# Kernel optimization log

Measured on AMD Instinct MI355X. Metric: run time of the kernel, lower is better.

Reference implementation:

```python
import jax, jax.numpy as jnp
import numpy as np

B, S, W = 64, 512, 16
E, TE, CE, CC = 300, 50, 50, 50
HID, TGT = 256, 16
VOCAB, TAGV, CHARV = 5002, 50, 100
IN = E + TE + CC  # 400


def setup_inputs() -> dict:
    key = jax.random.key(0)
    ks = jax.random.split(key, 24)
    sc = 0.1
    embed_table = (jax.random.normal(ks[0], (VOCAB, E)) * sc).at[0].set(0.0)
    tag_table = (jax.random.normal(ks[1], (TAGV, TE)) * sc).at[0].set(0.0)
    char_table = (jax.random.normal(ks[2], (CHARV, CE)) * sc).at[0].set(0.0)
    return {
        "X": jax.random.randint(ks[3], (B, S), 0, VOCAB),
        "labels_m": jax.random.uniform(ks[4], (B, S)),
        "tags": jax.random.randint(ks[5], (B, S), 0, TAGV),
        "chars": jax.random.randint(ks[6], (B, S, W), 0, CHARV),
        "embed_table": embed_table,
        "tag_table": tag_table,
        "char_table": char_table,
        "conv_w": jax.random.normal(ks[7], (CC, CE, 3)) * sc,
        "conv_b": jax.random.normal(ks[8], (CC,)) * sc,
        "w_ih_f": jax.random.normal(ks[9], (4 * HID, IN)) * sc,
        "w_hh_f": jax.random.normal(ks[10], (4 * HID, HID)) * sc,
        "b_ih_f": jax.random.normal(ks[11], (4 * HID,)) * sc,
        "b_hh_f": jax.random.normal(ks[12], (4 * HID,)) * sc,
        "w_ih_b": jax.random.normal(ks[13], (4 * HID, IN)) * sc,
        "w_hh_b": jax.random.normal(ks[14], (4 * HID, HID)) * sc,
        "b_ih_b": jax.random.normal(ks[15], (4 * HID,)) * sc,
        "b_hh_b": jax.random.normal(ks[16], (4 * HID,)) * sc,
        "fc_w": jax.random.normal(ks[17], (TGT, 2 * HID)) * sc,
        "fc_b": jax.random.normal(ks[18], (TGT,)) * sc,
        "A": jax.random.normal(ks[19], (TGT, TGT)),
        "wd": jax.random.normal(ks[20], (2 * HID,)),
    }


def _lstm_dir(xs, w_ih, w_hh, b_ih, b_hh, reverse):
    # xs: [S, B, IN] ; PyTorch gate order i,f,g,o
    h0 = jnp.zeros((xs.shape[1], w_hh.shape[1]), xs.dtype)

    def step(carry, x):
        h, c = carry
        g = x @ w_ih.T + h @ w_hh.T + (b_ih + b_hh)
        i, f, gg, o = jnp.split(g, 4, axis=-1)
        c = jax.nn.sigmoid(f) * c + jax.nn.sigmoid(i) * jnp.tanh(gg)
        h = jax.nn.sigmoid(o) * jnp.tanh(c)
        return (h, c), h

    _, hs = jax.lax.scan(step, (h0, h0), xs, reverse=reverse)
    return hs


def _features(X, labels_m, tags, chars, embed_table, tag_table, char_table,
              conv_w, conv_b, w_ih_f, w_hh_f, b_ih_f, b_hh_f,
              w_ih_b, w_hh_b, b_ih_b, b_hh_b, fc_w, fc_b, wd):
    embed = embed_table[X]          # [B,S,E]
    tag_embed = tag_table[tags]     # [B,S,TE]
    ce = char_table[chars]          # [B,S,W,CE]
    ce = ce.transpose(0, 3, 1, 2).reshape(B, CE, S * W)  # [B,CE,S*W]
    conv = jax.lax.conv_general_dilated(
        ce, conv_w, window_strides=(1,), padding=((1, 1),),
        dimension_numbers=("NCH", "OIH", "NCH")) + conv_b[None, :, None]
    char_conv = conv.reshape(B, CC, S, W).max(axis=3).transpose(0, 2, 1)  # [B,S,CC]
    feat = jnp.concatenate([embed, tag_embed, char_conv], axis=2)  # [B,S,IN]
    xs = feat.transpose(1, 0, 2)  # [S,B,IN]
    hf = _lstm_dir(xs, w_ih_f, w_hh_f, b_ih_f, b_hh_f, reverse=False)
    hb = _lstm_dir(xs, w_ih_b, w_hh_b, b_ih_b, b_hh_b, reverse=True)
    H = jnp.concatenate([hf, hb], axis=-1).transpose(1, 0, 2)  # [B,S,2H]
    H = H + labels_m[:, :, None] * wd[None, None, :]
    return H @ fc_w.T + fc_b  # [B,S,TGT]


def _viterbi(P, A):
    Xs = P.transpose(1, 0, 2)  # [S,B,T]
    b_idx = jnp.arange(P.shape[0])

    def vstep(delta, x):
        scores = delta[:, :, None] + A[None] + x[:, None, :]  # [B,prev,cur]
        return scores.max(axis=1), (scores.max(axis=1), scores.argmax(axis=1))

    deltaL, (drest, psis) = jax.lax.scan(vstep, Xs[0], Xs[1:])
    deltas = jnp.concatenate([Xs[0][None], drest], axis=0)  # [S,B,T]
    psi_end = deltaL.argmax(axis=1)                          # [B]
    score0 = deltaL[b_idx, psi_end]

    def back(carry, inp):
        tag, sc = carry
        psi_t, delta_t = inp
        prev = psi_t[b_idx, tag]
        return (prev, sc + delta_t[b_idx, prev]), prev

    (_, score), prevs = jax.lax.scan(back, (psi_end, score0),
                                     (psis, deltas[:-1]), reverse=True)
    path = jnp.concatenate([prevs, psi_end[None]], axis=0).T  # [B,S]
    return path, score


def reference(X, labels_m, tags, chars, embed_table, tag_table, char_table,
              conv_w, conv_b, w_ih_f, w_hh_f, b_ih_f, b_hh_f,
              w_ih_b, w_hh_b, b_ih_b, b_hh_b, fc_w, fc_b, A, wd):
    P = _features(X, labels_m, tags, chars, embed_table, tag_table, char_table,
                  conv_w, conv_b, w_ih_f, w_hh_f, b_ih_f, b_hh_f,
                  w_ih_b, w_hh_b, b_ih_b, b_hh_b, fc_w, fc_b, wd)
    return _viterbi(P, A)
```

## Files before the change

### kernel.cpp

```cpp
#include <hip/hip_runtime.h>


#define DEV __device__ __forceinline__
typedef unsigned short u16;
typedef unsigned int   u32;
typedef unsigned char  u8;
typedef signed char    s8;
using short8  = __attribute__((ext_vector_type(8))) short;
using f32x4   = __attribute__((ext_vector_type(4))) float;
using int4v   = __attribute__((ext_vector_type(4))) int;

DEV float bf2f(u16 u){ union{u32 i; float f;} v; v.i = ((u32)u)<<16; return v.f; }
DEV u16 f2bf(float f){ u32 x = __float_as_uint(f); return (u16)((x + 0x7fffu + ((x>>16)&1u)) >> 16); }
DEV float sigf(float x){ return __builtin_amdgcn_rcpf(1.f + __expf(-x)); }
DEV float tanh_f(float x){ return 1.f - 2.f*__builtin_amdgcn_rcpf(__expf(2.f*x) + 1.f); }
DEV float rdlane_f(float v, int l){
  return __uint_as_float(__builtin_amdgcn_readlane(__float_as_uint(v), l));
}

typedef __attribute__((address_space(1))) const u32 GU;
typedef __attribute__((address_space(3))) u32 LU;
DEV void gld_lds16(const void* g, void* l){
  __builtin_amdgcn_global_load_lds((GU*)g, (LU*)l, 16, 0, 0);
}
DEV void bar_l(){
  __builtin_amdgcn_sched_barrier(0);
  asm volatile("s_waitcnt lgkmcnt(0)" ::: "memory");
  __builtin_amdgcn_s_barrier();
  __builtin_amdgcn_sched_barrier(0);
}

static const size_t OFF_GI   = 0;
static const size_t OFF_P    = 0;
static const size_t OFF_DL   = OFF_P  + (size_t)32768*16*4;
static const size_t OFF_PSI  = OFF_DL + (size_t)32768*16*4;
static const size_t OFF_B    = (size_t)134217728;
static const size_t OFF_WIH  = OFF_B    + (size_t)33554432;
static const size_t OFF_WQ   = OFF_WIH  + (size_t)1703936;
static const size_t OFF_SC   = OFF_WQ   + (size_t)524288;
static const size_t OFF_BIAS = OFF_SC   + 8192;
static const size_t OFF_WFC  = OFF_BIAS + 8192;
static const size_t REQUIRED = OFF_WFC  + 256;

__global__ __launch_bounds__(256) void k0_all(
    const float* __restrict__ whhf, const float* __restrict__ whhb,
    s8* __restrict__ wq, float* __restrict__ sc2,
    const float* bihf, const float* bhhf, const float* bihb, const float* bhhb,
    const float* fcw, const float* wdp, float* bias, float* wfc,
    const float* __restrict__ wihf, const float* __restrict__ wihb, u16* __restrict__ wih)
{
  __shared__ float red[256];
  const int tid = threadIdx.x;
  const int bx = blockIdx.x;
  if (bx > 512){
    const int n = bx - 513;
    const float* src = (n < 1024) ? (wihf + (size_t)n*400) : (wihb + (size_t)(n-1024)*400);
    u32* dst = (u32*)(wih + (size_t)n*416);
    if (tid < 208){
      int j = tid*2;
      u32 v = 0u;
      if (j < 400){
        float2 f = *(const float2*)(src + j);
        v = (u32)f2bf(f.x) | ((u32)f2bf(f.y) << 16);
      }
      dst[tid] = v;
    }
    return;
  }
  if (bx == 512){
    for (int n = tid; n < 2048; n += 256){
      bias[n] = (n < 1024) ? (bihf[n] + bhhf[n]) : (bihb[n-1024] + bhhb[n-1024]);
    }
    const int cur = tid & 15, part = tid >> 4;
    float s = 0.f;
    for (int k = part*32; k < part*32 + 32; k++) s += fcw[cur*512 + k] * wdp[k];
    red[tid] = s;
    __syncthreads();
    if (tid < 16){
      float t = 0.f;
      #pragma unroll
      for (int p = 0; p < 16; p++) t += red[p*16 + tid];
      wfc[tid] = t;
    }
    return;
  }
  const int row = bx*4 + (tid >> 6);
  const int lane = tid & 63;
  const float* src = (row < 1024) ? (whhf + (size_t)row*256)
                                  : (whhb + (size_t)(row-1024)*256);
  f32x4 v = *(const f32x4*)(src + lane*4);
  float m = fmaxf(fmaxf(fabsf(v[0]), fabsf(v[1])), fmaxf(fabsf(v[2]), fabsf(v[3])));
  #pragma unroll
  for (int d = 1; d < 64; d <<= 1) m = fmaxf(m, __shfl_xor(m, d, 64));
  float inv = 127.f / (m + 1e-30f);
  u32 pack = 0;
  #pragma unroll
  for (int e = 0; e < 4; e++){
    int q = (int)rintf(v[e]*inv);
    q = q > 127 ? 127 : (q < -127 ? -127 : q);
    pack |= ((u32)(u8)(s8)q) << (8*e);
  }
  const int dir = row >> 10, n = row & 1023;
  const int g = n >> 8, j = n & 255, w2 = j >> 4, lr2 = j & 15;
  const int kk = lane >> 4, lq2 = (lane >> 2) & 3, e4 = lane & 3;
  u32* wq32 = (u32*)wq;
  wq32[dir*65536 + (((g*16 + w2)*4 + kk)*64 + lq2*16 + lr2)*4 + e4] = pack;
  if (lane == 0) sc2[row] = m * (1.f/16129.f);
}

__global__ __launch_bounds__(256) void k1_feat(
    const int* __restrict__ X, const int* __restrict__ tg, const int* __restrict__ ch,
    const float* __restrict__ etab, const float* __restrict__ ttab, const float* __restrict__ ctab,
    const float* __restrict__ cw, const float* __restrict__ cb, u16* __restrict__ feat)
{
  const int b = blockIdx.y, tid = threadIdx.x;
  __shared__ float ce_s[66*60];
  __shared__ float w_s[150*52];
  for (int i = tid; i < 7500; i += 256){
    int cc = i/150, r2 = i - cc*150;
    int ce = r2/3, dc = r2 - ce*3;
    w_s[(cc*3 + dc)*52 + ce] = cw[i];
  }
  const int li = tid & 15, jg = tid >> 4;

  for (int it = 0; it < 8; it++){
    const int sb = blockIdx.x*8 + it;
    __syncthreads();
    for (int i = tid; i < 600; i += 256){
      int wl = i/150, j = i - wl*150;
      int s = sb*4 + wl;
      int idx = X[b*512 + s];
      float2 f = *(const float2*)(etab + (size_t)idx*300 + j*2);
      *(u32*)(feat + (size_t)(s*64 + b)*416 + j*2) = (u32)f2bf(f.x) | ((u32)f2bf(f.y) << 16);
    }
    for (int i = tid; i < 100; i += 256){
      int wl = i/25, j = i - wl*25;
      int s = sb*4 + wl;
      int idx = tg[b*512 + s];
      float2 f = *(const float2*)(ttab + (size_t)idx*50 + j*2);
      *(u32*)(feat + (size_t)(s*64 + b)*416 + 300 + j*2) = (u32)f2bf(f.x) | ((u32)f2bf(f.y) << 16);
    }
    if (tid < 32){
      int wl = tid>>3, j = tid&7;
      int s = sb*4 + wl;
      *(u32*)(feat + (size_t)(s*64 + b)*416 + 400 + j*2) = 0u;
    }
    for (int i = tid; i < 3300; i += 256){
      int qq = i/50, ce = i - qq*50;
      int p = sb*64 - 1 + qq;
      float v = 0.f;
      if (p >= 0 && p < 8192){
        int ci = ch[b*8192 + p];
        v = ctab[ci*50 + ce];
      }
      ce_s[qq*60 + ce] = v;
    }
    __syncthreads();
    float acc[4][3];
    #pragma unroll
    for (int k=0;k<4;k++){ acc[k][0]=0.f; acc[k][1]=0.f; acc[k][2]=0.f; }
    #pragma unroll
    for (int dc = 0; dc < 3; dc++){
      for (int ceb = 0; ceb < 48; ceb += 4){
        f32x4 w0 = *(const f32x4*)&w_s[((3*jg+0)*3 + dc)*52 + ceb];
        f32x4 w1 = *(const f32x4*)&w_s[((3*jg+1)*3 + dc)*52 + ceb];
        f32x4 w2 = *(const f32x4*)&w_s[((3*jg+2)*3 + dc)*52 + ceb];
        #pragma unroll
        for (int k = 0; k < 4; k++){
          f32x4 cv = *(const f32x4*)&ce_s[(16*k + li + dc)*60 + ceb];
          #pragma unroll
          for (int e = 0; e < 4; e++){
            acc[k][0] += cv[e]*w0[e];
            acc[k][1] += cv[e]*w1[e];
            acc[k][2] += cv[e]*w2[e];
          }
        }
      }
      float w0a = w_s[((3*jg+0)*3+dc)*52 + 48], w0b = w_s[((3*jg+0)*3+dc)*52 + 49];
      float w1a = w_s[((3*jg+1)*3+dc)*52 + 48], w1b = w_s[((3*jg+1)*3+dc)*52 + 49];
      float w2a = w_s[((3*jg+2)*3+dc)*52 + 48], w2b = w_s[((3*jg+2)*3+dc)*52 + 49];
      #pragma unroll
      for (int k = 0; k < 4; k++){
        float ca = ce_s[(16*k + li + dc)*60 + 48];
        float cb2 = ce_s[(16*k + li + dc)*60 + 49];
        acc[k][0] += ca*w0a + cb2*w0b;
        acc[k][1] += ca*w1a + cb2*w1b;
        acc[k][2] += ca*w2a + cb2*w2b;
      }
    }
    #pragma unroll
    for (int m = 1; m < 16; m <<= 1)
      #pragma unroll
      for (int k=0;k<4;k++)
        #pragma unroll
        for (int c=0;c<3;c++)
          acc[k][c] = fmaxf(acc[k][c], __shfl_xor(acc[k][c], m, 64));
    if (li == 0){
      #pragma unroll
      for (int k=0;k<4;k++)
        #pragma unroll
        for (int c=0;c<3;c++){
          int cc = 3*jg + c;
          int s = sb*4 + k;
          feat[(size_t)(s*64 + b)*416 + 350 + cc] = f2bf(acc[k][c] + cb[cc]);
        }
    }
    if (tid < 128){
      int pl = tid & 63, cc = 48 + (tid >> 6);
      float a2 = 0.f;
      #pragma unroll
      for (int dc = 0; dc < 3; dc++){
        for (int ceb = 0; ceb < 48; ceb += 4){
          f32x4 wv = *(const f32x4*)&w_s[(cc*3 + dc)*52 + ceb];
          f32x4 cv = *(const f32x4*)&ce_s[(pl + dc)*60 + ceb];
          a2 += cv[0]*wv[0] + cv[1]*wv[1] + cv[2]*wv[2] + cv[3]*wv[3];
        }
        a2 += ce_s[(pl+dc)*60 + 48]*w_s[(cc*3+dc)*52 + 48]
            + ce_s[(pl+dc)*60 + 49]*w_s[(cc*3+dc)*52 + 49];
      }
      #pragma unroll
      for (int m = 1; m < 16; m <<= 1) a2 = fmaxf(a2, __shfl_xor(a2, m, 64));
      if ((tid & 15) == 0){
        int s = sb*4 + ((tid & 63) >> 4);
        feat[(size_t)(s*64 + b)*416 + 350 + cc] = f2bf(a2 + cb[cc]);
      }
    }
  }
}

__global__ __launch_bounds__(256) void k2_gemm(
    const u16* __restrict__ featp, const u16* __restrict__ wihp,
    const float* __restrict__ bias, u16* __restrict__ gi)
{
  const int m0 = blockIdx.y*128, n0 = blockIdx.x*128;
  const int tid = threadIdx.x, wv = tid>>6, lane = tid&63;
  const int lr = lane & 15, lq = lane >> 4;
  const int wm = (wv>>1)*64, wn = (wv&1)*64;
  __shared__ u16 As[2][4096], Bs[2][4096];
  f32x4 acc[4][4];
  #pragma unroll
  for (int a=0;a<4;a++)
    #pragma unroll
    for (int c=0;c<4;c++) acc[a][c] = (f32x4){0.f,0.f,0.f,0.f};

  const size_t arow = (size_t)(m0 + ((wv)*16) + (lane>>2))*416 + (lane&3)*8;
  const size_t brow = (size_t)(n0 + ((wv)*16) + (lane>>2))*416 + (lane&3)*8;
  #define K2_STAGE(BUF, K0) { \
    _Pragma("unroll") \
    for (int i = 0; i < 2; i++){ \
      int c = i*4 + wv; \
      gld_lds16(featp + (size_t)(m0 + c*16 + (lane>>2))*416 + (K0) + (lane&3)*8, &As[BUF][c*512]); \
      gld_lds16(wihp  + (size_t)(n0 + c*16 + (lane>>2))*416 + (K0) + (lane&3)*8, &Bs[BUF][c*512]); \
    } }

  K2_STAGE(0, 0);
  __syncthreads();
  int buf = 0;
  for (int ki = 0; ki < 13; ki++){
    if (ki < 12) K2_STAGE(buf^1, (ki+1)*32);
    short8 af[4], bfr[4];
    #pragma unroll
    for (int mt=0; mt<4; mt++) af[mt]  = *(const short8*)(&As[buf][0] + (wm + mt*16 + lr)*32 + lq*8);
    #pragma unroll
    for (int nt=0; nt<4; nt++) bfr[nt] = *(const short8*)(&Bs[buf][0] + (wn + nt*16 + lr)*32 + lq*8);
    #pragma unroll
    for (int mt=0; mt<4; mt++)
      #pragma unroll
      for (int nt=0; nt<4; nt++)
        acc[mt][nt] = __builtin_amdgcn_mfma_f32_16x16x32_bf16(af[mt], bfr[nt], acc[mt][nt], 0,0,0);
    __syncthreads();
    buf ^= 1;
  }
  #undef K2_STAGE
  (void)arow; (void)brow;
  #pragma unroll
  for (int nt=0; nt<4; nt++){
    float bv = bias[n0 + wn + nt*16 + lr];
    #pragma unroll
    for (int mt=0; mt<4; mt++)
      #pragma unroll
      for (int r=0; r<4; r++)
        gi[(size_t)(m0 + wm + mt*16 + lq*4 + r)*2048 + n0 + wn + nt*16 + lr]
            = f2bf(acc[mt][nt][r] + bv);
  }
}

__global__ __launch_bounds__(512, 2) void k3_lstm(
    const s8* __restrict__ wq, const float* __restrict__ sc2,
    const u16* __restrict__ gi, u16* __restrict__ hcat)
{
  const int dir = blockIdx.x >> 5;
  const int bb  = (blockIdx.x & 31) * 2;
  const int tid = threadIdx.x;
  const int w = tid >> 6, lane = tid & 63;
  const int lr = lane & 15, lq = lane >> 4;
  const int cb = tid >> 8, cj = tid & 255;

  __shared__ s8 Hs[2][4096];
  __shared__ float xbuf[2048];

  const s8* wqd = wq + dir*262144;
  int4v bq[2][4][4];
  #pragma unroll
  for (int sl = 0; sl < 2; sl++)
    #pragma unroll
    for (int g = 0; g < 4; g++)
      #pragma unroll
      for (int kk = 0; kk < 4; kk++)
        bq[sl][g][kk] = *(const int4v*)(wqd + (((((g*16 + 2*w + sl)*4 + kk)*64) + lane) << 4));

  float scl[4];
  #pragma unroll
  for (int g = 0; g < 4; g++) scl[g] = sc2[dir*1024 + g*256 + cj];

  *(uint2*)&Hs[0][tid*8] = (uint2){0u,0u};
  *(uint2*)&Hs[1][tid*8] = (uint2){0u,0u};

  float cst = 0.f;
  const ptrdiff_t dstep = dir ? -(ptrdiff_t)131072 : (ptrdiff_t)131072;
  const u16* g0 = gi + (size_t)((dir ? 511 : 0)*64 + bb + cb)*2048 + dir*1024 + cj;
  u32 gcur[4], gn1[4], gn2[4];
  #pragma unroll
  for (int g = 0; g < 4; g++) gcur[g] = g0[g*256];
  const u16* g1 = g0 + dstep;
  #pragma unroll
  for (int g = 0; g < 4; g++) gn1[g] = g1[g*256];
  const u16* gpref = g1;
  __syncthreads();

  #pragma unroll 1
  for (int t = 0; t < 512; t++){
    const int s = dir ? (511 - t) : t;
    if (t + 2 < 512) gpref += dstep;
    #pragma unroll
    for (int g = 0; g < 4; g++) gn2[g] = gpref[g*256];
    const s8* hb = Hs[t & 1];
    int4v aq[4];
    #pragma unroll
    for (int kk = 0; kk < 4; kk++)
      aq[kk] = *(const int4v*)(hb + lr*256 + ((kk*64 + lq*16) ^ (lr << 4)));
    int4v acc[2][4];
    #pragma unroll
    for (int sl = 0; sl < 2; sl++)
      #pragma unroll
      for (int g = 0; g < 4; g++) acc[sl][g] = (int4v){0,0,0,0};
    __builtin_amdgcn_s_setprio(1);
    #pragma unroll
    for (int kk = 0; kk < 4; kk++)
      #pragma unroll
      for (int sl = 0; sl < 2; sl++)
        #pragma unroll
        for (int g = 0; g < 4; g++)
          acc[sl][g] = __builtin_amdgcn_mfma_i32_16x16x64_i8(aq[kk], bq[sl][g][kk], acc[sl][g], 0,0,0);
    __builtin_amdgcn_s_setprio(0);
    if (lq == 0){
      #pragma unroll
      for (int sl = 0; sl < 2; sl++){
        const int j = (2*w + sl)*16 + lr;
        #pragma unroll
        for (int r = 0; r < 2; r++){
          f32x4 v = (f32x4){(float)acc[sl][0][r], (float)acc[sl][1][r],
                            (float)acc[sl][2][r], (float)acc[sl][3][r]};
          *(f32x4*)&xbuf[(r*256 + j)*4] = v;
        }
      }
    }
    bar_l();
    f32x4 p = *(const f32x4*)&xbuf[tid*4];
    float g4[4];
    #pragma unroll
    for (int g = 0; g < 4; g++) g4[g] = bf2f((u16)gcur[g]) + p[g]*scl[g];
    float iv = sigf(g4[0]), fv = sigf(g4[1]);
    float gg = tanh_f(g4[2]), ov = sigf(g4[3]);
    float c = fv*cst + iv*gg;
    cst = c;
    float h = ov * tanh_f(c);
    hcat[(size_t)(s*64 + bb + cb)*512 + dir*256 + cj] = f2bf(h);
    Hs[(t + 1) & 1][cb*256 + (cj ^ (cb << 4))] = (s8)(int)rintf(h * 127.f);
    #pragma unroll
    for (int g = 0; g < 4; g++){ gcur[g] = gn1[g]; gn1[g] = gn2[g]; }
    bar_l();
  }
}

__global__ __launch_bounds__(256) void k4_fc(
    const u16* __restrict__ hcat, const float* __restrict__ fcw, const float* __restrict__ fcb,
    const float* __restrict__ lmp, const float* __restrict__ wfc, float* __restrict__ Pout)
{
  const int wv = threadIdx.x >> 6, lane = threadIdx.x & 63;
  const int lr = lane & 15, lq = lane >> 4;
  const int mt = blockIdx.x*4 + wv;
  short8 bfr[16];
  #pragma unroll
  for (int kk = 0; kk < 16; kk++){
    const float* wr = fcw + (size_t)lr*512 + kk*32 + lq*8;
    f32x4 w0 = *(const f32x4*)wr;
    f32x4 w1 = *(const f32x4*)(wr + 4);
    short8 sv;
    #pragma unroll
    for (int e = 0; e < 4; e++){ sv[e] = (short)f2bf(w0[e]); sv[4+e] = (short)f2bf(w1[e]); }
    bfr[kk] = sv;
  }
  f32x4 acc = (f32x4){0.f,0.f,0.f,0.f};
  #pragma unroll
  for (int kk = 0; kk < 16; kk++){
    short8 af = *(const short8*)(hcat + (size_t)(mt*16 + lr)*512 + kk*32 + lq*8);
    acc = __builtin_amdgcn_mfma_f32_16x16x32_bf16(af, bfr[kk], acc, 0,0,0);
  }
  const int cur = lr;
  float fb = fcb[cur];
  float wf = wfc[cur];
  #pragma unroll
  for (int r = 0; r < 4; r++){
    int m = mt*16 + lq*4 + r;
    int b = m & 63, s = m >> 6;
    float lmv = lmp[b*512 + s];
    Pout[(size_t)m*16 + cur] = acc[r] + fb + lmv*wf;
  }
}

__global__ __launch_bounds__(64) void k5_vit(
    const float* __restrict__ Pg, const float* __restrict__ Am,
    float* __restrict__ dout, float* __restrict__ dl, u8* __restrict__ psi)
{
  const int b = blockIdx.x, lane = threadIdx.x;
  const int cur = lane & 15;
  float Ar[16];
  #pragma unroll
  for (int p = 0; p < 16; p++) Ar[p] = Am[p*16 + cur];
  float dreg[16];
  {
    float v0 = Pg[(size_t)b*16 + cur];
    if (lane < 16) dl[(size_t)b*16 + cur] = v0;
    #pragma unroll
    for (int c = 0; c < 16; c++) dreg[c] = rdlane_f(v0, c);
  }

#define FSTEP(X, S) { \
    float v_[16]; \
    _Pragma("unroll") \
    for (int p = 0; p < 16; p++) v_[p] = dreg[p] + Ar[p]; \
    float m1[8]; int i1[8]; \
    _Pragma("unroll") \
    for (int k = 0; k < 8; k++){ bool c_ = v_[2*k] >= v_[2*k+1]; \
      m1[k] = c_ ? v_[2*k] : v_[2*k+1]; i1[k] = c_ ? 2*k : 2*k+1; } \
    float m2[4]; int i2[4]; \
    _Pragma("unroll") \
    for (int k = 0; k < 4; k++){ bool c_ = m1[2*k] >= m1[2*k+1]; \
      m2[k] = c_ ? m1[2*k] : m1[2*k+1]; i2[k] = c_ ? i1[2*k] : i1[2*k+1]; } \
    float m3[2]; int i3[2]; \
    _Pragma("unroll") \
    for (int k = 0; k < 2; k++){ bool c_ = m2[2*k] >= m2[2*k+1]; \
      m3[k] = c_ ? m2[2*k] : m2[2*k+1]; i3[k] = c_ ? i2[2*k] : i2[2*k+1]; } \
    bool cf_ = m3[0] >= m3[1]; \
    float best = (cf_ ? m3[0] : m3[1]) + (X); \
    int bi = cf_ ? i3[0] : i3[1]; \
    if (lane < 16){ \
      dl[(size_t)((S)*64 + b)*16 + cur] = best; \
      psi[(size_t)((S)*64 + b)*16 + cur] = (u8)bi; \
    } \
    _Pragma("unroll") \
    for (int c = 0; c < 16; c++) dreg[c] = rdlane_f(best, c); \
  }

  float x0 = Pg[(size_t)(1*64 + b)*16 + cur];
  float x1 = Pg[(size_t)(2*64 + b)*16 + cur];
  float x2 = Pg[(size_t)(3*64 + b)*16 + cur];
  float x3 = Pg[(size_t)(4*64 + b)*16 + cur];
  for (int s = 1; s < 512; s += 4){
    FSTEP(x0, s);
    if (s + 4 < 512) x0 = Pg[(size_t)((s+4)*64 + b)*16 + cur];
    if (s + 1 < 512) FSTEP(x1, s+1);
    if (s + 5 < 512) x1 = Pg[(size_t)((s+5)*64 + b)*16 + cur];
    if (s + 2 < 512) FSTEP(x2, s+2);
    if (s + 6 < 512) x2 = Pg[(size_t)((s+6)*64 + b)*16 + cur];
    if (s + 3 < 512) FSTEP(x3, s+3);
    if (s + 7 < 512) x3 = Pg[(size_t)((s+7)*64 + b)*16 + cur];
  }
#undef FSTEP

  float bv = dreg[0]; int bix = 0;
  #pragma unroll
  for (int c = 1; c < 16; c++){ if (dreg[c] > bv){ bv = dreg[c]; bix = c; } }
  int tag = bix;
  float score = bv;
  if (lane == 0) dout[b*512 + 511] = (float)tag;

#define BSTEP(PV, DV, T) { \
    int prev = __builtin_amdgcn_readlane((PV), tag); \
    score += rdlane_f((DV), prev); \
    if (lane == 0) dout[b*512 + (T)] = (float)prev; \
    tag = prev; }

  int   p0 = 0, p1 = 0, p2 = 0, p3 = 0;
  float d0 = 0.f, d1 = 0.f, d2 = 0.f, d3 = 0.f;
  if (lane < 16){
    p0 = psi[(size_t)(511*64 + b)*16 + lane]; d0 = dl[(size_t)(510*64 + b)*16 + lane];
    p1 = psi[(size_t)(510*64 + b)*16 + lane]; d1 = dl[(size_t)(509*64 + b)*16 + lane];
    p2 = psi[(size_t)(509*64 + b)*16 + lane]; d2 = dl[(size_t)(508*64 + b)*16 + lane];
    p3 = psi[(size_t)(508*64 + b)*16 + lane]; d3 = dl[(size_t)(507*64 + b)*16 + lane];
  }
  for (int t = 510; t >= 0; t -= 4){
    BSTEP(p0, d0, t);
    if (t - 4 >= 0 && lane < 16){
      p0 = psi[(size_t)((t-3)*64 + b)*16 + lane]; d0 = dl[(size_t)((t-4)*64 + b)*16 + lane];
    }
    if (t - 1 >= 0) BSTEP(p1, d1, t-1);
    if (t - 5 >= 0 && lane < 16){
      p1 = psi[(size_t)((t-4)*64 + b)*16 + lane]; d1 = dl[(size_t)((t-5)*64 + b)*16 + lane];
    }
    if (t - 2 >= 0) BSTEP(p2, d2, t-2);
    if (t - 6 >= 0 && lane < 16){
      p2 = psi[(size_t)((t-5)*64 + b)*16 + lane]; d2 = dl[(size_t)((t-6)*64 + b)*16 + lane];
    }
    if (t - 3 >= 0) BSTEP(p3, d3, t-3);
    if (t - 7 >= 0 && lane < 16){
      p3 = psi[(size_t)((t-6)*64 + b)*16 + lane]; d3 = dl[(size_t)((t-7)*64 + b)*16 + lane];
    }
  }
#undef BSTEP
  if (lane == 0) dout[32768 + b] = score;
}

extern "C" void kernel_launch(void* const* d_in, const int* in_sizes, int n_in,
                              void* d_out, int out_size, void* d_ws, size_t ws_size,
                              hipStream_t stream)
{
  (void)in_sizes; (void)n_in; (void)out_size;
  if (ws_size < REQUIRED) return;

  const int*   X    = (const int*)d_in[0];
  const float* lm   = (const float*)d_in[1];
  const int*   tg   = (const int*)d_in[2];
  const int*   ch   = (const int*)d_in[3];
  const float* etab = (const float*)d_in[4];
  const float* ttab = (const float*)d_in[5];
  const float* ctab = (const float*)d_in[6];
  const float* cw   = (const float*)d_in[7];
  const float* cb   = (const float*)d_in[8];
  const float* wihf = (const float*)d_in[9];
  const float* whhf = (const float*)d_in[10];
  const float* bihf = (const float*)d_in[11];
  const float* bhhf = (const float*)d_in[12];
  const float* wihb = (const float*)d_in[13];
  const float* whhb = (const float*)d_in[14];
  const float* bihb = (const float*)d_in[15];
  const float* bhhb = (const float*)d_in[16];
  const float* fcw  = (const float*)d_in[17];
  const float* fcb  = (const float*)d_in[18];
  const float* Am   = (const float*)d_in[19];
  const float* wdp  = (const float*)d_in[20];

  char* ws = (char*)d_ws;
  u16*   gi   = (u16*)(ws + OFF_GI);
  u16*   feat = (u16*)(ws + OFF_B);
  u16*   hcat = (u16*)(ws + OFF_B);
  u16*   wih  = (u16*)(ws + OFF_WIH);
  s8*    wq   = (s8*)(ws + OFF_WQ);
  float* sc2  = (float*)(ws + OFF_SC);
  float* Pg   = (float*)(ws + OFF_P);
  float* dlt  = (float*)(ws + OFF_DL);
  u8*    psi  = (u8*)(ws + OFF_PSI);
  float* bias = (float*)(ws + OFF_BIAS);
  float* wfc  = (float*)(ws + OFF_WFC);
  float* dout = (float*)d_out;

  k0_all<<<2561, 256, 0, stream>>>(whhf, whhb, wq, sc2,
                                   bihf, bhhf, bihb, bhhb, fcw, wdp, bias, wfc,
                                   wihf, wihb, wih);
  k1_feat<<<dim3(16, 64), 256, 0, stream>>>(X, tg, ch, etab, ttab, ctab, cw, cb, feat);
  k2_gemm<<<dim3(16, 256), 256, 0, stream>>>(feat, wih, bias, gi);
  k3_lstm<<<64, 512, 0, stream>>>(wq, sc2, gi, hcat);
  k4_fc<<<512, 256, 0, stream>>>(hcat, fcw, fcb, lm, wfc, Pg);
  k5_vit<<<64, 64, 0, stream>>>(Pg, Am, dout, dlt, psi);
}
```

Before: 1.074 ms.

## Fuse weight prep and feature kernels; split embedding gather and prefetch char gathers

New measurement: 1.072 ms. About the same (-0.2%).

```diff
diff --git a/kernel.cpp b/kernel.cpp
--- a/kernel.cpp
+++ b/kernel.cpp
@@ -12,6 +12,7 @@
 
 DEV float bf2f(u16 u){ union{u32 i; float f;} v; v.i = ((u32)u)<<16; return v.f; }
 DEV u16 f2bf(float f){ u32 x = __float_as_uint(f); return (u16)((x + 0x7fffu + ((x>>16)&1u)) >> 16); }
+DEV u32 pk2(float a, float b){ return (u32)f2bf(a) | ((u32)f2bf(b) << 16); }
 DEV float sigf(float x){ return __builtin_amdgcn_rcpf(1.f + __expf(-x)); }
 DEV float tanh_f(float x){ return 1.f - 2.f*__builtin_amdgcn_rcpf(__expf(2.f*x) + 1.f); }
 DEV float rdlane_f(float v, int l){
@@ -42,16 +43,163 @@
 static const size_t OFF_WFC  = OFF_BIAS + 8192;
 static const size_t REQUIRED = OFF_WFC  + 256;
 
-__global__ __launch_bounds__(256) void k0_all(
+__global__ __launch_bounds__(256) void k01_fused(
+    const int* __restrict__ X, const int* __restrict__ tg, const int* __restrict__ ch,
+    const float* __restrict__ etab, const float* __restrict__ ttab, const float* __restrict__ ctab,
+    const float* __restrict__ cw, const float* __restrict__ cb, u16* __restrict__ feat,
     const float* __restrict__ whhf, const float* __restrict__ whhb,
     s8* __restrict__ wq, float* __restrict__ sc2,
     const float* bihf, const float* bhhf, const float* bihb, const float* bhhb,
     const float* fcw, const float* wdp, float* bias, float* wfc,
     const float* __restrict__ wihf, const float* __restrict__ wihb, u16* __restrict__ wih)
 {
-  __shared__ float red[256];
+  __shared__ float smem[3960 + 7800];
   const int tid = threadIdx.x;
-  const int bx = blockIdx.x;
+  const int bid = blockIdx.x;
+
+  if (bid < 1024){
+    float* ce_s = smem;
+    float* w_s  = smem + 3960;
+    const int b = bid >> 4, sbb = bid & 15;
+    for (int i = tid; i < 7500; i += 256){
+      int cc = i/150, r2 = i - cc*150;
+      int ce = r2/3, dc = r2 - ce*3;
+      w_s[(cc*3 + dc)*52 + ce] = cw[i];
+    }
+    const int li = tid & 15, jg = tid >> 4;
+    float stg[13];
+
+    #define GATHER(T) { \
+      const int sbg = sbb*8 + (T); \
+      _Pragma("unroll") \
+      for (int j = 0; j < 13; j++){ \
+        int i = tid + 256*j; \
+        float v = 0.f; \
+        if (i < 3300){ \
+          int qq = i/50, ce = i - qq*50; \
+          int p = sbg*64 - 1 + qq; \
+          if (p >= 0 && p < 8192){ int ci = ch[b*8192 + p]; v = ctab[ci*50 + ce]; } \
+        } \
+        stg[j] = v; \
+      } }
+
+    GATHER(0);
+    for (int t = 0; t < 8; t++){
+      const int sb = sbb*8 + t;
+      bar_l();
+      #pragma unroll
+      for (int j = 0; j < 13; j++){
+        int i = tid + 256*j;
+        if (i < 3300){
+          int qq = i/50, ce = i - qq*50;
+          ce_s[qq*60 + ce] = stg[j];
+        }
+      }
+      bar_l();
+      if (t < 7) GATHER(t+1);
+
+      float acc[4][3];
+      #pragma unroll
+      for (int k=0;k<4;k++){ acc[k][0]=0.f; acc[k][1]=0.f; acc[k][2]=0.f; }
+      #pragma unroll
+      for (int dc = 0; dc < 3; dc++){
+        for (int ceb = 0; ceb < 48; ceb += 4){
+          f32x4 w0 = *(const f32x4*)&w_s[((3*jg+0)*3 + dc)*52 + ceb];
+          f32x4 w1 = *(const f32x4*)&w_s[((3*jg+1)*3 + dc)*52 + ceb];
+          f32x4 w2 = *(const f32x4*)&w_s[((3*jg+2)*3 + dc)*52 + ceb];
+          #pragma unroll
+          for (int k = 0; k < 4; k++){
+            f32x4 cv = *(const f32x4*)&ce_s[(16*k + li + dc)*60 + ceb];
+            #pragma unroll
+            for (int e = 0; e < 4; e++){
+              acc[k][0] += cv[e]*w0[e];
+              acc[k][1] += cv[e]*w1[e];
+              acc[k][2] += cv[e]*w2[e];
+            }
+          }
+        }
+        float w0a = w_s[((3*jg+0)*3+dc)*52 + 48], w0b = w_s[((3*jg+0)*3+dc)*52 + 49];
+        float w1a = w_s[((3*jg+1)*3+dc)*52 + 48], w1b = w_s[((3*jg+1)*3+dc)*52 + 49];
+        float w2a = w_s[((3*jg+2)*3+dc)*52 + 48], w2b = w_s[((3*jg+2)*3+dc)*52 + 49];
+        #pragma unroll
+        for (int k = 0; k < 4; k++){
+          float ca  = ce_s[(16*k + li + dc)*60 + 48];
+          float cb2 = ce_s[(16*k + li + dc)*60 + 49];
+          acc[k][0] += ca*w0a + cb2*w0b;
+          acc[k][1] += ca*w1a + cb2*w1b;
+          acc[k][2] += ca*w2a + cb2*w2b;
+        }
+      }
+      #pragma unroll
+      for (int m = 1; m < 16; m <<= 1)
+        #pragma unroll
+        for (int k=0;k<4;k++)
+          #pragma unroll
+          for (int c=0;c<3;c++)
+            acc[k][c] = fmaxf(acc[k][c], __shfl_xor(acc[k][c], m, 64));
+      if (li == 0){
+        #pragma unroll
+        for (int k=0;k<4;k++)
+          #pragma unroll
+          for (int c=0;c<3;c++){
+            int cc = 3*jg + c;
+            int s = sb*4 + k;
+            feat[(size_t)(s*64 + b)*416 + 350 + cc] = f2bf(acc[k][c] + cb[cc]);
+          }
+      }
+      if (tid < 128){
+        int pl = tid & 63, cc = 48 + (tid >> 6);
+        float a2 = 0.f;
+        #pragma unroll
+        for (int dc = 0; dc < 3; dc++){
+          for (int ceb = 0; ceb < 48; ceb += 4){
+            f32x4 wv = *(const f32x4*)&w_s[(cc*3 + dc)*52 + ceb];
+            f32x4 cv = *(const f32x4*)&ce_s[(pl + dc)*60 + ceb];
+            a2 += cv[0]*wv[0] + cv[1]*wv[1] + cv[2]*wv[2] + cv[3]*wv[3];
+          }
+          a2 += ce_s[(pl+dc)*60 + 48]*w_s[(cc*3+dc)*52 + 48]
+              + ce_s[(pl+dc)*60 + 49]*w_s[(cc*3+dc)*52 + 49];
+        }
+        #pragma unroll
+        for (int m = 1; m < 16; m <<= 1) a2 = fmaxf(a2, __shfl_xor(a2, m, 64));
+        if ((tid & 15) == 0){
+          int s = sb*4 + ((tid & 63) >> 4);
+          feat[(size_t)(s*64 + b)*416 + 350 + cc] = f2bf(a2 + cb[cc]);
+        }
+      }
+    }
+    #undef GATHER
+    return;
+  }
+
+  if (bid < 3072){
+    const int cid = bid - 1024;
+    const int w = tid >> 6, lane = tid & 63;
+    #pragma unroll
+    for (int r = 0; r < 4; r++){
+      const int m = cid*16 + w*4 + r;
+      const int s = m >> 6, b = m & 63;
+      const int xi = X[b*512 + s];
+      const int ti = tg[b*512 + s];
+      u32* dst = (u32*)feat + (size_t)m*208;
+      #pragma unroll
+      for (int pass = 0; pass < 3; pass++){
+        int word = pass*64 + lane;
+        if (word < 150){
+          float2 f = *(const float2*)(etab + (size_t)xi*300 + word*2);
+          dst[word] = pk2(f.x, f.y);
+        } else if (word < 175){
+          float2 f = *(const float2*)(ttab + (size_t)ti*50 + (word-150)*2);
+          dst[word] = pk2(f.x, f.y);
+        } else if (word < 183){
+          dst[200 + word - 175] = 0u;
+        }
+      }
+    }
+    return;
+  }
+
+  const int bx = bid - 3072;
   if (bx > 512){
     const int n = bx - 513;
     const float* src = (n < 1024) ? (wihf + (size_t)n*400) : (wihb + (size_t)(n-1024)*400);
@@ -61,13 +209,14 @@
       u32 v = 0u;
       if (j < 400){
         float2 f = *(const float2*)(src + j);
-        v = (u32)f2bf(f.x) | ((u32)f2bf(f.y) << 16);
+        v = pk2(f.x, f.y);
       }
       dst[tid] = v;
     }
     return;
   }
   if (bx == 512){
+    float* red = smem;
     for (int n = tid; n < 2048; n += 256){
       bias[n] = (n < 1024) ? (bihf[n] + bhhf[n]) : (bihb[n-1024] + bhhb[n-1024]);
     }
@@ -84,147 +233,29 @@
     }
     return;
   }
-  const int row = bx*4 + (tid >> 6);
-  const int lane = tid & 63;
-  const float* src = (row < 1024) ? (whhf + (size_t)row*256)
-                                  : (whhb + (size_t)(row-1024)*256);
-  f32x4 v = *(const f32x4*)(src + lane*4);
-  float m = fmaxf(fmaxf(fabsf(v[0]), fabsf(v[1])), fmaxf(fabsf(v[2]), fabsf(v[3])));
-  #pragma unroll
-  for (int d = 1; d < 64; d <<= 1) m = fmaxf(m, __shfl_xor(m, d, 64));
-  float inv = 127.f / (m + 1e-30f);
-  u32 pack = 0;
-  #pragma unroll
-  for (int e = 0; e < 4; e++){
-    int q = (int)rintf(v[e]*inv);
-    q = q > 127 ? 127 : (q < -127 ? -127 : q);
-    pack |= ((u32)(u8)(s8)q) << (8*e);
-  }
-  const int dir = row >> 10, n = row & 1023;
-  const int g = n >> 8, j = n & 255, w2 = j >> 4, lr2 = j & 15;
-  const int kk = lane >> 4, lq2 = (lane >> 2) & 3, e4 = lane & 3;
-  u32* wq32 = (u32*)wq;
-  wq32[dir*65536 + (((g*16 + w2)*4 + kk)*64 + lq2*16 + lr2)*4 + e4] = pack;
-  if (lane == 0) sc2[row] = m * (1.f/16129.f);
-}
-
-__global__ __launch_bounds__(256) void k1_feat(
-    const int* __restrict__ X, const int* __restrict__ tg, const int* __restrict__ ch,
-    const float* __restrict__ etab, const float* __restrict__ ttab, const float* __restrict__ ctab,
-    const float* __restrict__ cw, const float* __restrict__ cb, u16* __restrict__ feat)
-{
-  const int b = blockIdx.y, tid = threadIdx.x;
-  __shared__ float ce_s[66*60];
-  __shared__ float w_s[150*52];
-  for (int i = tid; i < 7500; i += 256){
-    int cc = i/150, r2 = i - cc*150;
-    int ce = r2/3, dc = r2 - ce*3;
-    w_s[(cc*3 + dc)*52 + ce] = cw[i];
-  }
-  const int li = tid & 15, jg = tid >> 4;
-
-  for (int it = 0; it < 8; it++){
-    const int sb = blockIdx.x*8 + it;
-    __syncthreads();
-    for (int i = tid; i < 600; i += 256){
-      int wl = i/150, j = i - wl*150;
-      int s = sb*4 + wl;
-      int idx = X[b*512 + s];
-      float2 f = *(const float2*)(etab + (size_t)idx*300 + j*2);
-      *(u32*)(feat + (size_t)(s*64 + b)*416 + j*2) = (u32)f2bf(f.x) | ((u32)f2bf(f.y) << 16);
-    }
-    for (int i = tid; i < 100; i += 256){
-      int wl = i/25, j = i - wl*25;
-      int s = sb*4 + wl;
-      int idx = tg[b*512 + s];
-      float2 f = *(const float2*)(ttab + (size_t)idx*50 + j*2);
-      *(u32*)(feat + (size_t)(s*64 + b)*416 + 300 + j*2) = (u32)f2bf(f.x) | ((u32)f2bf(f.y) << 16);
-    }
-    if (tid < 32){
-      int wl = tid>>3, j = tid&7;
-      int s = sb*4 + wl;
-      *(u32*)(feat + (size_t)(s*64 + b)*416 + 400 + j*2) = 0u;
-    }
-    for (int i = tid; i < 3300; i += 256){
-      int qq = i/50, ce = i - qq*50;
-      int p = sb*64 - 1 + qq;
-      float v = 0.f;
-      if (p >= 0 && p < 8192){
-        int ci = ch[b*8192 + p];
-        v = ctab[ci*50 + ce];
-      }
-      ce_s[qq*60 + ce] = v;
-    }
-    __syncthreads();
-    float acc[4][3];
-    #pragma unroll
-    for (int k=0;k<4;k++){ acc[k][0]=0.f; acc[k][1]=0.f; acc[k][2]=0.f; }
-    #pragma unroll
-    for (int dc = 0; dc < 3; dc++){
-      for (int ceb = 0; ceb < 48; ceb += 4){
-        f32x4 w0 = *(const f32x4*)&w_s[((3*jg+0)*3 + dc)*52 + ceb];
-        f32x4 w1 = *(const f32x4*)&w_s[((3*jg+1)*3 + dc)*52 + ceb];
-        f32x4 w2 = *(const f32x4*)&w_s[((3*jg+2)*3 + dc)*52 + ceb];
-        #pragma unroll
-        for (int k = 0; k < 4; k++){
-          f32x4 cv = *(const f32x4*)&ce_s[(16*k + li + dc)*60 + ceb];
-          #pragma unroll
-          for (int e = 0; e < 4; e++){
-            acc[k][0] += cv[e]*w0[e];
-            acc[k][1] += cv[e]*w1[e];
-            acc[k][2] += cv[e]*w2[e];
-          }
-        }
-      }
-      float w0a = w_s[((3*jg+0)*3+dc)*52 + 48], w0b = w_s[((3*jg+0)*3+dc)*52 + 49];
-      float w1a = w_s[((3*jg+1)*3+dc)*52 + 48], w1b = w_s[((3*jg+1)*3+dc)*52 + 49];
-      float w2a = w_s[((3*jg+2)*3+dc)*52 + 48], w2b = w_s[((3*jg+2)*3+dc)*52 + 49];
-      #pragma unroll
-      for (int k = 0; k < 4; k++){
-        float ca = ce_s[(16*k + li + dc)*60 + 48];
-        float cb2 = ce_s[(16*k + li + dc)*60 + 49];
-        acc[k][0] += ca*w0a + cb2*w0b;
-        acc[k][1] += ca*w1a + cb2*w1b;
-        acc[k][2] += ca*w2a + cb2*w2b;
-      }
-    }
-    #pragma unroll
-    for (int m = 1; m < 16; m <<= 1)
-      #pragma unroll
-      for (int k=0;k<4;k++)
-        #pragma unroll
-        for (int c=0;c<3;c++)
-          acc[k][c] = fmaxf(acc[k][c], __shfl_xor(acc[k][c], m, 64));
-    if (li == 0){
-      #pragma unroll
-      for (int k=0;k<4;k++)
-        #pragma unroll
-        for (int c=0;c<3;c++){
-          int cc = 3*jg + c;
-          int s = sb*4 + k;
-          feat[(size_t)(s*64 + b)*416 + 350 + cc] = f2bf(acc[k][c] + cb[cc]);
-        }
-    }
-    if (tid < 128){
-      int pl = tid & 63, cc = 48 + (tid >> 6);
-      float a2 = 0.f;
-      #pragma unroll
-      for (int dc = 0; dc < 3; dc++){
-        for (int ceb = 0; ceb < 48; ceb += 4){
-          f32x4 wv = *(const f32x4*)&w_s[(cc*3 + dc)*52 + ceb];
-          f32x4 cv = *(const f32x4*)&ce_s[(pl + dc)*60 + ceb];
-          a2 += cv[0]*wv[0] + cv[1]*wv[1] + cv[2]*wv[2] + cv[3]*wv[3];
-        }
-        a2 += ce_s[(pl+dc)*60 + 48]*w_s[(cc*3+dc)*52 + 48]
-            + ce_s[(pl+dc)*60 + 49]*w_s[(cc*3+dc)*52 + 49];
-      }
-      #pragma unroll
-      for (int m = 1; m < 16; m <<= 1) a2 = fmaxf(a2, __shfl_xor(a2, m, 64));
-      if ((tid & 15) == 0){
-        int s = sb*4 + ((tid & 63) >> 4);
-        feat[(size_t)(s*64 + b)*416 + 350 + cc] = f2bf(a2 + cb[cc]);
-      }
-    }
+  {
+    const int row = bx*4 + (tid >> 6);
+    const int lane = tid & 63;
+    const float* src = (row < 1024) ? (whhf + (size_t)row*256)
+                                    : (whhb + (size_t)(row-1024)*256);
+    f32x4 v = *(const f32x4*)(src + lane*4);
+    float m = fmaxf(fmaxf(fabsf(v[0]), fabsf(v[1])), fmaxf(fabsf(v[2]), fabsf(v[3])));
+    #pragma unroll
+    for (int d = 1; d < 64; d <<= 1) m = fmaxf(m, __shfl_xor(m, d, 64));
+    float inv = 127.f / (m + 1e-30f);
+    u32 pack = 0;
+    #pragma unroll
+    for (int e = 0; e < 4; e++){
+      int q = (int)rintf(v[e]*inv);
+      q = q > 127 ? 127 : (q < -127 ? -127 : q);
+      pack |= ((u32)(u8)(s8)q) << (8*e);
+    }
+    const int dir = row >> 10, n = row & 1023;
+    const int g = n >> 8, j = n & 255, w2 = j >> 4, lr2 = j & 15;
+    const int kk = lane >> 4, lq2 = (lane >> 2) & 3, e4 = lane & 3;
+    u32* wq32 = (u32*)wq;
+    wq32[dir*65536 + (((g*16 + w2)*4 + kk)*64 + lq2*16 + lr2)*4 + e4] = pack;
+    if (lane == 0) sc2[row] = m * (1.f/16129.f);
   }
 }
 
@@ -243,8 +274,6 @@
     #pragma unroll
     for (int c=0;c<4;c++) acc[a][c] = (f32x4){0.f,0.f,0.f,0.f};
 
-  const size_t arow = (size_t)(m0 + ((wv)*16) + (lane>>2))*416 + (lane&3)*8;
-  const size_t brow = (size_t)(n0 + ((wv)*16) + (lane>>2))*416 + (lane&3)*8;
   #define K2_STAGE(BUF, K0) { \
     _Pragma("unroll") \
     for (int i = 0; i < 2; i++){ \
@@ -272,7 +301,6 @@
     buf ^= 1;
   }
   #undef K2_STAGE
-  (void)arow; (void)brow;
   #pragma unroll
   for (int nt=0; nt<4; nt++){
     float bv = bias[n0 + wn + nt*16 + lr];
@@ -565,10 +593,10 @@
   float* wfc  = (float*)(ws + OFF_WFC);
   float* dout = (float*)d_out;
 
-  k0_all<<<2561, 256, 0, stream>>>(whhf, whhb, wq, sc2,
-                                   bihf, bhhf, bihb, bhhb, fcw, wdp, bias, wfc,
-                                   wihf, wihb, wih);
-  k1_feat<<<dim3(16, 64), 256, 0, stream>>>(X, tg, ch, etab, ttab, ctab, cw, cb, feat);
+  k01_fused<<<5633, 256, 0, stream>>>(X, tg, ch, etab, ttab, ctab, cw, cb, feat,
+                                      whhf, whhb, wq, sc2,
+                                      bihf, bhhf, bihb, bhhb, fcw, wdp, bias, wfc,
+                                      wihf, wihb, wih);
   k2_gemm<<<dim3(16, 256), 256, 0, stream>>>(feat, wih, bias, gi);
   k3_lstm<<<64, 512, 0, stream>>>(wq, sc2, gi, hcat);
   k4_fc<<<512, 256, 0, stream>>>(hcat, fcw, fcb, lm, wfc, Pg);
```
